# Performance work log

Measured on AMD Instinct MI355X. Metric: run time of the kernel, lower is better.

## Reference

```python
import jax, jax.numpy as jnp
import numpy as np

B, S, D, H = 2, 2048, 1024, 16
DK = D // H  # 64, per-head key/value dim


def setup_inputs() -> dict:
    key = jax.random.key(0)
    ks = jax.random.split(key, 8)
    q = jax.random.normal(ks[0], (B, S, D), dtype=jnp.float32)
    k = jax.random.normal(ks[1], (B, S, D), dtype=jnp.float32)
    v = jax.random.normal(ks[2], (B, S, D), dtype=jnp.float32)
    # per-head projection weights, initialized like torch.randn in the original
    W_q = jax.random.normal(ks[3], (H, D, DK), dtype=jnp.float32)
    W_k = jax.random.normal(ks[4], (H, D, DK), dtype=jnp.float32)
    W_v = jax.random.normal(ks[5], (H, D, DK), dtype=jnp.float32)
    # output nn.Linear(H*DK, D): weight [D, H*DK], bias [D]
    bound = 1.0 / np.sqrt(H * DK)
    W_o = jax.random.uniform(ks[6], (D, H * DK), dtype=jnp.float32, minval=-bound, maxval=bound)
    b_o = jax.random.uniform(ks[7], (D,), dtype=jnp.float32, minval=-bound, maxval=bound)
    return {"q": q, "k": k, "v": v, "W_q": W_q, "W_k": W_k, "W_v": W_v, "W_o": W_o, "b_o": b_o}


def reference(q, k, v, W_q, W_k, W_v, W_o, b_o):
    dk = W_q.shape[-1]
    # batched per-head projections (replaces the Python loop over heads)
    qh = jnp.einsum('bsd,hdk->bhsk', q, W_q)  # [B,H,S,DK]
    kh = jnp.einsum('bsd,hdk->bhsk', k, W_k)
    vh = jnp.einsum('bsd,hdk->bhsk', v, W_v)
    scale = jnp.asarray(np.sqrt(dk), qh.dtype)
    scores = jnp.einsum('bhsk,bhtk->bhst', qh, kh) / scale  # [B,H,S,S]
    attn = jax.nn.softmax(scores, axis=-1)
    ctx = jnp.einsum('bhst,bhtk->bhsk', attn, vh)  # [B,H,S,DK]
    # concat heads along feature dim (matches torch.cat(..., dim=2))
    b, h, s, d = ctx.shape
    ctx = ctx.transpose(0, 2, 1, 3).reshape(b, s, h * d)  # [B,S,H*DK]
    return ctx @ W_o.T + b_o  # [B,S,D]
```

## Files before the change

kernel.cpp:

```cpp
#include <hip/hip_runtime.h>
#include <math.h>

#define B_ 2
#define S_ 2048
#define D_ 1024
#define H_ 16
#define ATTN_C 0.18033688011f

typedef unsigned short ushort_t;
typedef __attribute__((ext_vector_type(8))) short short8;
typedef __attribute__((ext_vector_type(4))) short short4v;
typedef __attribute__((ext_vector_type(4))) float f32x4;
typedef __attribute__((ext_vector_type(2))) float f32x2;
typedef __attribute__((ext_vector_type(16))) float f32x16;
typedef __attribute__((ext_vector_type(4))) unsigned int uint4v;

#define MFMA(A, B, C) __builtin_amdgcn_mfma_f32_32x32x16_bf16((A), (B), (C), 0, 0, 0)
#define Z16 {0.f,0.f,0.f,0.f,0.f,0.f,0.f,0.f,0.f,0.f,0.f,0.f,0.f,0.f,0.f,0.f}

__device__ __forceinline__ ushort_t bf16rn(float x) {
    unsigned int u = __builtin_bit_cast(unsigned int, x);
    u += 0x7FFFu + ((u >> 16) & 1u);
    return (ushort_t)(u >> 16);
}
__device__ __forceinline__ float bf16tof(ushort_t h) {
    return __builtin_bit_cast(float, (unsigned int)h << 16);
}
__device__ __forceinline__ unsigned cvtpk(float lo, float hi) {
    unsigned r;
    asm("v_cvt_pk_bf16_f32 %0, %1, %2" : "=v"(r) : "v"(lo), "v"(hi));
    return r;
}
__device__ __forceinline__ void gload16(const void* g, void* l) {
    __builtin_amdgcn_global_load_lds(
        (const __attribute__((address_space(1))) unsigned int*)(unsigned long long)g,
        (__attribute__((address_space(3))) unsigned int*)(unsigned int)(unsigned long long)l,
        16, 0, 0);
}

__global__ __launch_bounds__(256) void cvtx_kernel(
    const float* __restrict__ Xq, const float* __restrict__ Xk,
    const float* __restrict__ Xv,
    ushort_t* __restrict__ Xh, ushort_t* __restrict__ Xl)
{
    const int pr = blockIdx.y;
    const float* X = pr == 0 ? Xq : pr == 1 ? Xk : Xv;
    const size_t idx = ((size_t)blockIdx.x * 256 + threadIdx.x) * 8;
    f32x4 v0 = *(const f32x4*)(X + idx);
    f32x4 v1 = *(const f32x4*)(X + idx + 4);
    float f[8] = {v0.x, v0.y, v0.z, v0.w, v1.x, v1.y, v1.z, v1.w};
    short8 hi, lo;
#pragma unroll
    for (int i = 0; i < 8; ++i) {
        ushort_t hh = bf16rn(f[i]);
        hi[i] = (short)hh;
        lo[i] = (short)bf16rn(f[i] - bf16tof(hh));
    }
    const size_t base = (size_t)pr * 2 * S_ * D_;
    *(short8*)(Xh + base + idx) = hi;
    if (pr < 2) *(short8*)(Xl + base + idx) = lo;
}

__global__ __launch_bounds__(256) void cvtw_kernel(
    const float* __restrict__ Wq, const float* __restrict__ Wk,
    const float* __restrict__ Wv,
    ushort_t* __restrict__ wqh, ushort_t* __restrict__ wql,
    ushort_t* __restrict__ wkh, ushort_t* __restrict__ wkl,
    ushort_t* __restrict__ wvh)
{
    __shared__ float T[64][68];
    const int dt = blockIdx.x, h = blockIdx.y, mat = blockIdx.z;
    const int tid = threadIdx.x;
    const float* W = mat == 0 ? Wq : mat == 1 ? Wk : Wv;
    const float* Wb = W + ((size_t)h * 1024 + dt * 64) * 64;
#pragma unroll
    for (int u = 0; u < 4; ++u) {
        int idx = tid + u * 256;
        int d = idx >> 4, c4 = idx & 15;
        f32x4 v = *(const f32x4*)(Wb + (size_t)d * 64 + c4 * 4);
        T[d][c4 * 4 + 0] = v.x; T[d][c4 * 4 + 1] = v.y;
        T[d][c4 * 4 + 2] = v.z; T[d][c4 * 4 + 3] = v.w;
    }
    __syncthreads();
    ushort_t* oh = mat == 0 ? wqh : mat == 1 ? wkh : wvh;
    ushort_t* ol = mat == 0 ? wql : mat == 1 ? wkl : nullptr;
#pragma unroll
    for (int u = 0; u < 4; ++u) {
        int idx = tid + u * 256;
        int n = idx >> 4, c4 = idx & 15;
        float v0 = T[c4 * 4 + 0][n], v1 = T[c4 * 4 + 1][n];
        float v2 = T[c4 * 4 + 2][n], v3 = T[c4 * 4 + 3][n];
        ushort_t h0 = bf16rn(v0), h1 = bf16rn(v1), h2 = bf16rn(v2), h3 = bf16rn(v3);
        size_t off = ((size_t)h * 64 + n) * 1024 + dt * 64 + c4 * 4;
        short4v hv = {(short)h0, (short)h1, (short)h2, (short)h3};
        *(short4v*)(oh + off) = hv;
        if (ol) {
            short4v lv = {(short)bf16rn(v0 - bf16tof(h0)), (short)bf16rn(v1 - bf16tof(h1)),
                          (short)bf16rn(v2 - bf16tof(h2)), (short)bf16rn(v3 - bf16tof(h3))};
            *(short4v*)(ol + off) = lv;
        }
    }
}

__global__ __launch_bounds__(256) void cvtwo_kernel(
    const float* __restrict__ Wo, ushort_t* __restrict__ wob)
{
    size_t idx = (size_t)blockIdx.x * 256 + threadIdx.x;
    f32x4 v = *(const f32x4*)(Wo + idx * 4);
    short4v o = {(short)bf16rn(v.x), (short)bf16rn(v.y),
                 (short)bf16rn(v.z), (short)bf16rn(v.w)};
    *(short4v*)(wob + idx * 4) = o;
}

__global__ __launch_bounds__(256, 2) void proj_kernel(
    const ushort_t* __restrict__ Xh, const ushort_t* __restrict__ Xl,
    const ushort_t* __restrict__ Wh_q, const ushort_t* __restrict__ Wl_q,
    const ushort_t* __restrict__ Wh_k, const ushort_t* __restrict__ Wl_k,
    const ushort_t* __restrict__ Wh_v,
    ushort_t* __restrict__ Oq_h, ushort_t* __restrict__ Oq_l,
    ushort_t* __restrict__ Ok_h, ushort_t* __restrict__ Ok_l,
    ushort_t* __restrict__ Ov)
{
    __shared__ __align__(16) ushort_t Xs[128 * 128];
    __shared__ __align__(16) ushort_t Ws[128 * 128];
    const int tid = threadIdx.x;
    const int wv = tid >> 6, lane = tid & 63;
    const int lo32 = lane & 31, g = lane >> 5;
    const int wm = wv >> 1, wn = wv & 1;
    const int lrow = lane >> 4, lg = lane & 15;
    const int m0 = blockIdx.x * 128;
    const int n0 = blockIdx.y * 128;
    const int pr = blockIdx.z >> 1, b = blockIdx.z & 1;
    const bool split = (pr != 2);
    const ushort_t* Whp = pr == 0 ? Wh_q : pr == 1 ? Wh_k : Wh_v;
    const ushort_t* Wlp = pr == 0 ? Wl_q : pr == 1 ? Wl_k : Wh_v;
    const ushort_t* Xhb = Xh + ((size_t)(pr * 2 + b) * S_ + m0) * D_;
    const ushort_t* Xlb = Xl + ((size_t)(pr * 2 + b) * S_ + m0) * D_;
    f32x16 a00 = Z16, a01 = Z16, a10 = Z16, a11 = Z16;

    for (int d0 = 0; d0 < D_; d0 += 64) {
        __syncthreads();
#pragma unroll
        for (int u = 0; u < 8; ++u) {
            int row = u * 16 + wv * 4 + lrow;
            int gs = lg ^ (row & 15);
            int half = gs >> 3, c8 = gs & 7;
            const ushort_t* srcX = ((half && split) ? Xlb : Xhb) + (size_t)row * D_ + d0 + c8 * 8;
            gload16(srcX, (char*)Xs + (u * 16 + wv * 4) * 256);
            const ushort_t* srcW = ((half && split) ? Wlp : Whp) + (size_t)(n0 + row) * 1024 + d0 + c8 * 8;
            gload16(srcW, (char*)Ws + (u * 16 + wv * 4) * 256);
        }
        __syncthreads();
#pragma unroll
        for (int ks = 0; ks < 4; ++ks) {
            int coff = ks * 16 + g * 8;
            int r0 = wm * 64 + lo32, r1 = r0 + 32;
            int c0 = wn * 64 + lo32, c1 = c0 + 32;
            short8 a0h = *(const short8*)&Xs[(r0 * 128 + coff) ^ ((r0 & 15) << 3)];
            short8 a1h = *(const short8*)&Xs[(r1 * 128 + coff) ^ ((r1 & 15) << 3)];
            short8 b0h = *(const short8*)&Ws[(c0 * 128 + coff) ^ ((c0 & 15) << 3)];
            short8 b1h = *(const short8*)&Ws[(c1 * 128 + coff) ^ ((c1 & 15) << 3)];
            a00 = MFMA(a0h, b0h, a00);
            a01 = MFMA(a0h, b1h, a01);
            a10 = MFMA(a1h, b0h, a10);
            a11 = MFMA(a1h, b1h, a11);
            if (split) {
                short8 a0l = *(const short8*)&Xs[(r0 * 128 + 64 + coff) ^ ((r0 & 15) << 3)];
                short8 a1l = *(const short8*)&Xs[(r1 * 128 + 64 + coff) ^ ((r1 & 15) << 3)];
                short8 b0l = *(const short8*)&Ws[(c0 * 128 + 64 + coff) ^ ((c0 & 15) << 3)];
                short8 b1l = *(const short8*)&Ws[(c1 * 128 + 64 + coff) ^ ((c1 & 15) << 3)];
                a00 = MFMA(a0h, b0l, a00); a00 = MFMA(a0l, b0h, a00);
                a01 = MFMA(a0h, b1l, a01); a01 = MFMA(a0l, b1h, a01);
                a10 = MFMA(a1h, b0l, a10); a10 = MFMA(a1l, b0h, a10);
                a11 = MFMA(a1h, b1l, a11); a11 = MFMA(a1l, b1h, a11);
            }
        }
    }
    ushort_t* OH = pr == 0 ? Oq_h : pr == 1 ? Ok_h : Ov;
    ushort_t* OL = pr == 0 ? Oq_l : pr == 1 ? Ok_l : Ov;
    const bool qscale = (pr == 0);
#define PROJ_STORE(ACC, MT, NT)                                               \
    _Pragma("unroll")                                                         \
    for (int r = 0; r < 16; ++r) {                                            \
        int s_loc = m0 + wm * 64 + (MT) * 32 + (r & 3) + 8 * (r >> 2) + 4 * g;\
        int col = n0 + wn * 64 + (NT) * 32 + lo32;                            \
        int hh_ = col >> 6, nn = col & 63;                                    \
        float val = ACC[r];                                                   \
        if (qscale) val *= ATTN_C;                                            \
        size_t off = (((size_t)b * H_ + hh_) * S_ + s_loc) * 64 + nn;         \
        if (split) {                                                          \
            ushort_t hv = bf16rn(val);                                        \
            OH[off] = hv;                                                     \
            OL[off] = bf16rn(val - bf16tof(hv));                              \
        } else OH[off] = bf16rn(val);                                         \
    }
    PROJ_STORE(a00, 0, 0)
    PROJ_STORE(a01, 0, 1)
    PROJ_STORE(a10, 1, 0)
    PROJ_STORE(a11, 1, 1)
#undef PROJ_STORE
}

__global__ __launch_bounds__(256, 4) void attn_kernel(
    const ushort_t* __restrict__ qh_h, const ushort_t* __restrict__ qh_l,
    const ushort_t* __restrict__ kh_h, const ushort_t* __restrict__ kh_l,
    const ushort_t* __restrict__ vh, ushort_t* __restrict__ Opart,
    float* __restrict__ Ml)
{
    __shared__ __align__(16) char smem[32768];
    ushort_t* Ks = (ushort_t*)smem;
    ushort_t* Vt = (ushort_t*)(smem + 16384);
    const int tid = threadIdx.x;
    const int wv = tid >> 6, lane = tid & 63;
    const int lo32 = lane & 31, g = lane >> 5;
    const int lrow = lane >> 4, lg = lane & 15;
    const int s0 = blockIdx.x * 128;
    const int h = blockIdx.y;
    const int b = blockIdx.z >> 1, sp = blockIdx.z & 1;
    const size_t bhs = ((size_t)b * H_ + h) * S_ * 64;

    const ushort_t* Qrh = qh_h + bhs + (size_t)(s0 + wv * 32 + lo32) * 64;
    const ushort_t* Qrl = qh_l + bhs + (size_t)(s0 + wv * 32 + lo32) * 64;
    short8 qfh[4], qfl[4];
#pragma unroll
    for (int ks = 0; ks < 4; ++ks) {
        qfh[ks] = *(const short8*)(Qrh + ks * 16 + g * 8);
        qfl[ks] = *(const short8*)(Qrl + ks * 16 + g * 8);
    }
    const ushort_t* Kgh = kh_h + bhs;
    const ushort_t* Kgl = kh_l + bhs;
    const ushort_t* Vg = vh + bhs;

    f32x16 o0 = Z16, o1 = Z16;
    float mrun = -3.0e38f, lrun = 0.0f;
    const int kvbeg = sp * (S_ / 2), kvend = kvbeg + (S_ / 2);

    for (int kv0 = kvbeg; kv0 < kvend; kv0 += 64) {
        __syncthreads();
#pragma unroll
        for (int u = 0; u < 4; ++u) {
            int row = wv * 16 + u * 4 + lrow;
            int gs = lg ^ (row & 15);
            int half = gs >> 3, c8 = gs & 7;
            const ushort_t* src = (half ? Kgl : Kgh) + (size_t)(kv0 + row) * 64 + c8 * 8;
            gload16(src, (char*)Ks + (wv * 16 + u * 4) * 256);
        }
        {
            int kvp = tid & 31, d8 = tid >> 5;
            const ushort_t* vp = Vg + (size_t)(kv0 + 2 * kvp) * 64 + d8 * 8;
            short8 va = *(const short8*)(vp);
            short8 vb = *(const short8*)(vp + 64);
#pragma unroll
            for (int i = 0; i < 8; ++i) {
                int d = d8 * 8 + i;
                unsigned wrd = ((unsigned)(ushort_t)vb[i] << 16) | (ushort_t)va[i];
                *(unsigned*)&Vt[(d * 64 + 2 * kvp) ^ ((d & 7) << 3)] = wrd;
            }
        }
        __syncthreads();
#pragma unroll
        for (int ch = 0; ch < 2; ++ch) {
            int kvb = ch * 32;
            f32x16 st = Z16;
#pragma unroll
            for (int ks = 0; ks < 4; ++ks) {
                int krow = kvb + lo32;
                int base = krow * 128 + ks * 16 + g * 8;
                int sw = (krow & 15) << 3;
                short8 kfh = *(const short8*)&Ks[base ^ sw];
                short8 kfl = *(const short8*)&Ks[(base + 64) ^ sw];
                st = MFMA(kfh, qfh[ks], st);
                st = MFMA(kfh, qfl[ks], st);
                st = MFMA(kfl, qfh[ks], st);
            }
            float t0 = fmaxf(fmaxf(st[0], st[1]), st[2]);
            float t1 = fmaxf(fmaxf(st[3], st[4]), st[5]);
            float t2 = fmaxf(fmaxf(st[6], st[7]), st[8]);
            float t3 = fmaxf(fmaxf(st[9], st[10]), st[11]);
            float t4 = fmaxf(fmaxf(st[12], st[13]), st[14]);
            float cmax = fmaxf(fmaxf(fmaxf(t0, t1), t2),
                               fmaxf(fmaxf(t3, t4), st[15]));
            cmax = fmaxf(cmax, __shfl_xor(cmax, 32));
            if (!__all(cmax <= mrun)) {
                float mnew = fmaxf(mrun, cmax);
                float corr = __builtin_amdgcn_exp2f(mrun - mnew);
                lrun *= corr;
#pragma unroll
                for (int r = 0; r < 16; ++r) { o0[r] *= corr; o1[r] *= corr; }
                mrun = mnew;
            }
            float p[16];
            float ls = 0.f;
#pragma unroll
            for (int r = 0; r < 16; ++r) {
                p[r] = __builtin_amdgcn_exp2f(st[r] - mrun);
                ls += p[r];
            }
            lrun += ls;
#pragma unroll
            for (int ks2 = 0; ks2 < 2; ++ks2) {
                int rr = ks2 * 8;
                unsigned w0 = cvtpk(p[rr + 0], p[rr + 1]);
                unsigned w1 = cvtpk(p[rr + 2], p[rr + 3]);
                unsigned w2 = cvtpk(p[rr + 4], p[rr + 5]);
                unsigned w3 = cvtpk(p[rr + 6], p[rr + 7]);
                asm("v_permlane32_swap_b32 %0, %1" : "+v"(w0), "+v"(w2));
                asm("v_permlane32_swap_b32 %0, %1" : "+v"(w1), "+v"(w3));
                uint4v pw = {w0, w1, w2, w3};
                short8 pfrag = __builtin_bit_cast(short8, pw);
                int kvf = kvb + ks2 * 16 + g * 8;
                int vsw = (lo32 & 7) << 3;
                short8 vf0 = *(const short8*)&Vt[(lo32 * 64 + kvf) ^ vsw];
                short8 vf1 = *(const short8*)&Vt[((lo32 + 32) * 64 + kvf) ^ vsw];
                o0 = MFMA(vf0, pfrag, o0);
                o1 = MFMA(vf1, pfrag, o1);
            }
        }
    }
    lrun += __shfl_xor(lrun, 32);
    __syncthreads();
    float* Oe = ((float*)smem) + wv * 2048;
#pragma unroll
    for (int r = 0; r < 16; ++r) {
        int dd = (r & 3) + 8 * (r >> 2) + 4 * g;
        int qsw = (lo32 & 7) << 2;
        Oe[(lo32 * 64 + dd) ^ qsw] = o0[r];
        Oe[(lo32 * 64 + 32 + dd) ^ qsw] = o1[r];
    }
    const size_t orow = (size_t)sp * (B_ * H_ * S_) + ((size_t)b * H_ + h) * S_ + s0 + wv * 32;
#pragma unroll
    for (int rep = 0; rep < 8; ++rep) {
        int idx = lane + rep * 64;
        int qq = idx >> 4, d4 = idx & 15;
        f32x4 ov = *(const f32x4*)&Oe[(qq * 64 + d4 * 4) ^ ((qq & 7) << 2)];
        short4v pk4 = {(short)bf16rn(ov.x), (short)bf16rn(ov.y),
                       (short)bf16rn(ov.z), (short)bf16rn(ov.w)};
        *(short4v*)(Opart + (orow + qq) * 64 + d4 * 4) = pk4;
    }
    if (g == 0) {
        f32x2 ml = {mrun, lrun};
        *(f32x2*)(Ml + (orow + lo32) * 2) = ml;
    }
}

__global__ __launch_bounds__(256) void merge_kernel(
    const ushort_t* __restrict__ Opart, const float* __restrict__ Ml,
    ushort_t* __restrict__ ctxb)
{
    const int NROW = B_ * H_ * S_;
    int gidx = blockIdx.x * 256 + threadIdx.x;
    int row = gidx >> 3, d8 = (gidx & 7) * 8;
    f32x2 ml0 = *(const f32x2*)(Ml + (size_t)row * 2);
    f32x2 ml1 = *(const f32x2*)(Ml + ((size_t)NROW + row) * 2);
    float M = fmaxf(ml0.x, ml1.x);
    float w0 = __builtin_amdgcn_exp2f(ml0.x - M);
    float w1 = __builtin_amdgcn_exp2f(ml1.x - M);
    float inv = 1.f / (ml0.y * w0 + ml1.y * w1);
    w0 *= inv; w1 *= inv;
    short8 a = *(const short8*)(Opart + (size_t)row * 64 + d8);
    short8 c = *(const short8*)(Opart + ((size_t)NROW + row) * 64 + d8);
    short8 o;
#pragma unroll
    for (int i = 0; i < 8; ++i) {
        float f = bf16tof((ushort_t)a[i]) * w0 + bf16tof((ushort_t)c[i]) * w1;
        o[i] = (short)bf16rn(f);
    }
    int bb = row >> 15, hh = (row >> 11) & 15, s = row & 2047;
    *(short8*)(ctxb + ((size_t)bb * S_ + s) * D_ + hh * 64 + d8) = o;
}

__global__ __launch_bounds__(128, 2) void outproj_kernel(
    const ushort_t* __restrict__ ctxb, const ushort_t* __restrict__ wob,
    const float* __restrict__ bo, float* __restrict__ Out)
{
    __shared__ __align__(16) ushort_t Cs[128 * 128];
    __shared__ __align__(16) ushort_t Ws2[64 * 128];
    const int tid = threadIdx.x;
    const int wv = tid >> 6, lane = tid & 63;
    const int lo32 = lane & 31, g = lane >> 5;
    const int lrow = lane >> 4, lg = lane & 15;
    const int n0 = blockIdx.x * 64;
    const int m0 = blockIdx.y * 128;
    f32x16 a00 = Z16, a01 = Z16, a10 = Z16, a11 = Z16;
    for (int k0 = 0; k0 < D_; k0 += 128) {
        __syncthreads();
#pragma unroll
        for (int u = 0; u < 16; ++u) {
            int row = u * 8 + wv * 4 + lrow;
            int gs = lg ^ (row & 15);
            const ushort_t* src = ctxb + (size_t)(m0 + row) * D_ + k0 + gs * 8;
            gload16(src, (char*)Cs + (u * 8 + wv * 4) * 256);
        }
#pragma unroll
        for (int u = 0; u < 8; ++u) {
            int row = u * 8 + wv * 4 + lrow;
            int gs = lg ^ (row & 15);
            const ushort_t* src = wob + (size_t)(n0 + row) * D_ + k0 + gs * 8;
            gload16(src, (char*)Ws2 + (u * 8 + wv * 4) * 256);
        }
        __syncthreads();
#pragma unroll
        for (int ks = 0; ks < 8; ++ks) {
            int coff = ks * 16 + g * 8;
            int r0 = wv * 64 + lo32, r1 = r0 + 32;
            int n1 = lo32 + 32;
            short8 A0 = *(const short8*)&Cs[(r0 * 128 + coff) ^ ((r0 & 15) << 3)];
            short8 A1 = *(const short8*)&Cs[(r1 * 128 + coff) ^ ((r1 & 15) << 3)];
            short8 B0 = *(const short8*)&Ws2[(lo32 * 128 + coff) ^ ((lo32 & 15) << 3)];
            short8 B1 = *(const short8*)&Ws2[(n1 * 128 + coff) ^ ((n1 & 15) << 3)];
            a00 = MFMA(A0, B0, a00);
            a01 = MFMA(A0, B1, a01);
            a10 = MFMA(A1, B0, a10);
            a11 = MFMA(A1, B1, a11);
        }
    }
    float b0v = bo[n0 + lo32], b1v = bo[n0 + 32 + lo32];
#define OUT_STORE(ACC, MT, NT, BV)                                          \
    _Pragma("unroll")                                                       \
    for (int r = 0; r < 16; ++r) {                                          \
        int m = m0 + wv * 64 + (MT) * 32 + (r & 3) + 8 * (r >> 2) + 4 * g;  \
        int n = n0 + (NT) * 32 + lo32;                                      \
        Out[(size_t)m * D_ + n] = ACC[r] + (BV);                            \
    }
    OUT_STORE(a00, 0, 0, b0v)
    OUT_STORE(a01, 0, 1, b1v)
    OUT_STORE(a10, 1, 0, b0v)
    OUT_STORE(a11, 1, 1, b1v)
#undef OUT_STORE
}

extern "C" void kernel_launch(void* const* d_in, const int* in_sizes, int n_in,
                              void* d_out, int out_size, void* d_ws,
                              size_t ws_size, hipStream_t stream)
{
    const float* q = (const float*)d_in[0];
    const float* k = (const float*)d_in[1];
    const float* v = (const float*)d_in[2];
    const float* W_q = (const float*)d_in[3];
    const float* W_k = (const float*)d_in[4];
    const float* W_v = (const float*)d_in[5];
    const float* W_o = (const float*)d_in[6];
    const float* b_o = (const float*)d_in[7];
    float* out = (float*)d_out;

    ushort_t* wqt_h = (ushort_t*)d_ws;
    ushort_t* wqt_l = wqt_h + (1 << 20);
    ushort_t* wkt_h = wqt_l + (1 << 20);
    ushort_t* wkt_l = wkt_h + (1 << 20);
    ushort_t* wvt_h = wkt_l + (1 << 20);
    ushort_t* wob   = wvt_h + (1 << 20);
    ushort_t* qh_h  = wob + (1 << 20);
    ushort_t* qh_l  = qh_h + (1 << 22);
    ushort_t* kh_h  = qh_l + (1 << 22);
    ushort_t* kh_l  = kh_h + (1 << 22);
    ushort_t* vhp   = kh_l + (1 << 22);
    ushort_t* Xh    = vhp + (1 << 22);
    ushort_t* Xl    = Xh + 3 * (1 << 22);
    ushort_t* ctxb  = Xh;
    ushort_t* Opart = Xl;
    float*    Ml    = (float*)(Xl + 2 * (size_t)(B_ * H_ * S_) * 64);

    cvtx_kernel<<<dim3(2048, 3), 256, 0, stream>>>(q, k, v, Xh, Xl);
    cvtw_kernel<<<dim3(16, 16, 3), 256, 0, stream>>>(
        W_q, W_k, W_v, wqt_h, wqt_l, wkt_h, wkt_l, wvt_h);
    cvtwo_kernel<<<1024, 256, 0, stream>>>(W_o, wob);
    proj_kernel<<<dim3(16, 8, 6), 256, 0, stream>>>(
        Xh, Xl, wqt_h, wqt_l, wkt_h, wkt_l, wvt_h,
        qh_h, qh_l, kh_h, kh_l, vhp);
    attn_kernel<<<dim3(16, 16, 4), 256, 0, stream>>>(
        qh_h, qh_l, kh_h, kh_l, vhp, Opart, Ml);
    merge_kernel<<<2048, 256, 0, stream>>>(Opart, Ml, ctxb);
    outproj_kernel<<<dim3(16, 32), 128, 0, stream>>>(ctxb, wob, b_o, out);
}
```

Before: 224.3 us.

## Widen attention tiles, pre-transpose V in projection, skip negligible score chunks

The projection kernel now writes V directly in a transposed [d][s] layout, so the attention kernel can load it with async 16-byte copies instead of transposing it through registers. Each wave now handles 64 query rows (two 32-row fragments) against 128-key tiles. Each key fragment is reused across two query fragments, and synchronisation is amortised over more work, at the cost of fewer blocks per CU and more registers. A chunk is skipped when its high-part-only scores are all at least 142 below the running max. Otherwise the low-part correction MFMAs run only for the query fragments that need them, avoiding exp and PV work whose contribution underflows.

```diff
diff --git a/kernel.cpp b/kernel.cpp
--- a/kernel.cpp
+++ b/kernel.cpp
@@ -119,7 +119,7 @@
     const ushort_t* __restrict__ Wh_v,
     ushort_t* __restrict__ Oq_h, ushort_t* __restrict__ Oq_l,
     ushort_t* __restrict__ Ok_h, ushort_t* __restrict__ Ok_l,
-    ushort_t* __restrict__ Ov)
+    ushort_t* __restrict__ Ovt)
 {
     __shared__ __align__(16) ushort_t Xs[128 * 128];
     __shared__ __align__(16) ushort_t Ws[128 * 128];
@@ -176,8 +176,8 @@
             }
         }
     }
-    ushort_t* OH = pr == 0 ? Oq_h : pr == 1 ? Ok_h : Ov;
-    ushort_t* OL = pr == 0 ? Oq_l : pr == 1 ? Ok_l : Ov;
+    ushort_t* OH = pr == 0 ? Oq_h : pr == 1 ? Ok_h : Ovt;
+    ushort_t* OL = pr == 0 ? Oq_l : pr == 1 ? Ok_l : Ovt;
     const bool qscale = (pr == 0);
 #define PROJ_STORE(ACC, MT, NT)                                               \
     _Pragma("unroll")                                                         \
@@ -187,12 +187,15 @@
         int hh_ = col >> 6, nn = col & 63;                                    \
         float val = ACC[r];                                                   \
         if (qscale) val *= ATTN_C;                                            \
-        size_t off = (((size_t)b * H_ + hh_) * S_ + s_loc) * 64 + nn;         \
         if (split) {                                                          \
+            size_t off = (((size_t)b * H_ + hh_) * S_ + s_loc) * 64 + nn;     \
             ushort_t hv = bf16rn(val);                                        \
             OH[off] = hv;                                                     \
             OL[off] = bf16rn(val - bf16tof(hv));                              \
-        } else OH[off] = bf16rn(val);                                         \
+        } else {                                                              \
+            size_t offt = (((size_t)b * H_ + hh_) * 64 + nn) * S_ + s_loc;    \
+            OH[offt] = bf16rn(val);                                           \
+        }                                                                     \
     }
     PROJ_STORE(a00, 0, 0)
     PROJ_STORE(a01, 0, 1)
@@ -201,133 +204,203 @@
 #undef PROJ_STORE
 }
 
-__global__ __launch_bounds__(256, 4) void attn_kernel(
+__global__ __launch_bounds__(256, 2) void attn_kernel(
     const ushort_t* __restrict__ qh_h, const ushort_t* __restrict__ qh_l,
     const ushort_t* __restrict__ kh_h, const ushort_t* __restrict__ kh_l,
-    const ushort_t* __restrict__ vh, ushort_t* __restrict__ Opart,
+    const ushort_t* __restrict__ vt, ushort_t* __restrict__ Opart,
     float* __restrict__ Ml)
 {
-    __shared__ __align__(16) char smem[32768];
+    __shared__ __align__(16) char smem[49152];
     ushort_t* Ks = (ushort_t*)smem;
-    ushort_t* Vt = (ushort_t*)(smem + 16384);
+    ushort_t* Vt = (ushort_t*)(smem + 32768);
     const int tid = threadIdx.x;
     const int wv = tid >> 6, lane = tid & 63;
     const int lo32 = lane & 31, g = lane >> 5;
     const int lrow = lane >> 4, lg = lane & 15;
-    const int s0 = blockIdx.x * 128;
+    const int s0 = blockIdx.x * 256;
     const int h = blockIdx.y;
     const int b = blockIdx.z >> 1, sp = blockIdx.z & 1;
     const size_t bhs = ((size_t)b * H_ + h) * S_ * 64;
 
-    const ushort_t* Qrh = qh_h + bhs + (size_t)(s0 + wv * 32 + lo32) * 64;
-    const ushort_t* Qrl = qh_l + bhs + (size_t)(s0 + wv * 32 + lo32) * 64;
-    short8 qfh[4], qfl[4];
-#pragma unroll
-    for (int ks = 0; ks < 4; ++ks) {
-        qfh[ks] = *(const short8*)(Qrh + ks * 16 + g * 8);
-        qfl[ks] = *(const short8*)(Qrl + ks * 16 + g * 8);
+    short8 qfh[2][4], qfl[2][4];
+#pragma unroll
+    for (int c = 0; c < 2; ++c) {
+        const ushort_t* Qrh = qh_h + bhs + (size_t)(s0 + wv * 64 + c * 32 + lo32) * 64;
+        const ushort_t* Qrl = qh_l + bhs + (size_t)(s0 + wv * 64 + c * 32 + lo32) * 64;
+#pragma unroll
+        for (int ks = 0; ks < 4; ++ks) {
+            qfh[c][ks] = *(const short8*)(Qrh + ks * 16 + g * 8);
+            qfl[c][ks] = *(const short8*)(Qrl + ks * 16 + g * 8);
+        }
     }
     const ushort_t* Kgh = kh_h + bhs;
     const ushort_t* Kgl = kh_l + bhs;
-    const ushort_t* Vg = vh + bhs;
-
-    f32x16 o0 = Z16, o1 = Z16;
-    float mrun = -3.0e38f, lrun = 0.0f;
+    const ushort_t* Vtg = vt + ((size_t)b * H_ + h) * 64 * S_;
+
+    f32x16 o00 = Z16, o01 = Z16, o10 = Z16, o11 = Z16;
+    float mrun0 = -3.0e38f, mrun1 = -3.0e38f;
+    float lrun0 = 0.f, lrun1 = 0.f;
     const int kvbeg = sp * (S_ / 2), kvend = kvbeg + (S_ / 2);
 
-    for (int kv0 = kvbeg; kv0 < kvend; kv0 += 64) {
+    for (int kv0 = kvbeg; kv0 < kvend; kv0 += 128) {
         __syncthreads();
 #pragma unroll
-        for (int u = 0; u < 4; ++u) {
-            int row = wv * 16 + u * 4 + lrow;
+        for (int u = 0; u < 8; ++u) {
+            int row = u * 16 + wv * 4 + lrow;
             int gs = lg ^ (row & 15);
             int half = gs >> 3, c8 = gs & 7;
             const ushort_t* src = (half ? Kgl : Kgh) + (size_t)(kv0 + row) * 64 + c8 * 8;
-            gload16(src, (char*)Ks + (wv * 16 + u * 4) * 256);
-        }
-        {
-            int kvp = tid & 31, d8 = tid >> 5;
-            const ushort_t* vp = Vg + (size_t)(kv0 + 2 * kvp) * 64 + d8 * 8;
-            short8 va = *(const short8*)(vp);
-            short8 vb = *(const short8*)(vp + 64);
-#pragma unroll
-            for (int i = 0; i < 8; ++i) {
-                int d = d8 * 8 + i;
-                unsigned wrd = ((unsigned)(ushort_t)vb[i] << 16) | (ushort_t)va[i];
-                *(unsigned*)&Vt[(d * 64 + 2 * kvp) ^ ((d & 7) << 3)] = wrd;
+            gload16(src, (char*)Ks + (u * 16 + wv * 4) * 256);
+        }
+#pragma unroll
+        for (int u = 0; u < 4; ++u) {
+            int d = u * 16 + wv * 4 + lrow;
+            int gsrc = (lg & 8) | ((lg & 7) ^ (d & 7));
+            const ushort_t* src = Vtg + (size_t)d * S_ + kv0 + gsrc * 8;
+            gload16(src, (char*)Vt + (u * 16 + wv * 4) * 256);
+        }
+        __syncthreads();
+#pragma unroll 1
+        for (int ch = 0; ch < 4; ++ch) {
+            const int kvb = ch * 32;
+            const int krow = kvb + lo32;
+            const int ksw = (krow & 15) << 3;
+            short8 kfh0 = *(const short8*)&Ks[(krow * 128 + 0 * 16 + g * 8) ^ ksw];
+            short8 kfh1 = *(const short8*)&Ks[(krow * 128 + 1 * 16 + g * 8) ^ ksw];
+            short8 kfh2 = *(const short8*)&Ks[(krow * 128 + 2 * 16 + g * 8) ^ ksw];
+            short8 kfh3 = *(const short8*)&Ks[(krow * 128 + 3 * 16 + g * 8) ^ ksw];
+            f32x16 st0 = Z16, st1 = Z16;
+            st0 = MFMA(kfh0, qfh[0][0], st0);  st1 = MFMA(kfh0, qfh[1][0], st1);
+            st0 = MFMA(kfh1, qfh[0][1], st0);  st1 = MFMA(kfh1, qfh[1][1], st1);
+            st0 = MFMA(kfh2, qfh[0][2], st0);  st1 = MFMA(kfh2, qfh[1][2], st1);
+            st0 = MFMA(kfh3, qfh[0][3], st0);  st1 = MFMA(kfh3, qfh[1][3], st1);
+            float cm0 = fmaxf(fmaxf(fmaxf(st0[0], st0[1]), fmaxf(st0[2], st0[3])),
+                              fmaxf(fmaxf(st0[4], st0[5]), fmaxf(st0[6], st0[7])));
+            cm0 = fmaxf(cm0, fmaxf(fmaxf(fmaxf(st0[8], st0[9]), fmaxf(st0[10], st0[11])),
+                                   fmaxf(fmaxf(st0[12], st0[13]), fmaxf(st0[14], st0[15]))));
+            float cm1 = fmaxf(fmaxf(fmaxf(st1[0], st1[1]), fmaxf(st1[2], st1[3])),
+                              fmaxf(fmaxf(st1[4], st1[5]), fmaxf(st1[6], st1[7])));
+            cm1 = fmaxf(cm1, fmaxf(fmaxf(fmaxf(st1[8], st1[9]), fmaxf(st1[10], st1[11])),
+                                   fmaxf(fmaxf(st1[12], st1[13]), fmaxf(st1[14], st1[15]))));
+            cm0 = fmaxf(cm0, __shfl_xor(cm0, 32));
+            cm1 = fmaxf(cm1, __shfl_xor(cm1, 32));
+            const bool need0 = !__all(cm0 <= mrun0 - 142.f);
+            const bool need1 = !__all(cm1 <= mrun1 - 142.f);
+            if (!need0 && !need1) continue;
+            short8 kfl0 = *(const short8*)&Ks[(krow * 128 + 64 + 0 * 16 + g * 8) ^ ksw];
+            short8 kfl1 = *(const short8*)&Ks[(krow * 128 + 64 + 1 * 16 + g * 8) ^ ksw];
+            short8 kfl2 = *(const short8*)&Ks[(krow * 128 + 64 + 2 * 16 + g * 8) ^ ksw];
+            short8 kfl3 = *(const short8*)&Ks[(krow * 128 + 64 + 3 * 16 + g * 8) ^ ksw];
+            unsigned pw0[8], pw1[8];
+            if (need0) {
+                st0 = MFMA(kfh0, qfl[0][0], st0);  st0 = MFMA(kfl0, qfh[0][0], st0);
+                st0 = MFMA(kfh1, qfl[0][1], st0);  st0 = MFMA(kfl1, qfh[0][1], st0);
+                st0 = MFMA(kfh2, qfl[0][2], st0);  st0 = MFMA(kfl2, qfh[0][2], st0);
+                st0 = MFMA(kfh3, qfl[0][3], st0);  st0 = MFMA(kfl3, qfh[0][3], st0);
+                float cme = fmaxf(fmaxf(fmaxf(st0[0], st0[1]), fmaxf(st0[2], st0[3])),
+                                  fmaxf(fmaxf(st0[4], st0[5]), fmaxf(st0[6], st0[7])));
+                cme = fmaxf(cme, fmaxf(fmaxf(fmaxf(st0[8], st0[9]), fmaxf(st0[10], st0[11])),
+                                       fmaxf(fmaxf(st0[12], st0[13]), fmaxf(st0[14], st0[15]))));
+                cme = fmaxf(cme, __shfl_xor(cme, 32));
+                if (!__all(cme <= mrun0)) {
+                    float mnew = fmaxf(mrun0, cme);
+                    float corr = __builtin_amdgcn_exp2f(mrun0 - mnew);
+                    lrun0 *= corr;
+#pragma unroll
+                    for (int r = 0; r < 16; ++r) { o00[r] *= corr; o01[r] *= corr; }
+                    mrun0 = mnew;
+                }
+                float p[16], ls = 0.f;
+#pragma unroll
+                for (int r = 0; r < 16; ++r) {
+                    p[r] = __builtin_amdgcn_exp2f(st0[r] - mrun0);
+                    ls += p[r];
+                }
+                lrun0 += ls;
+#pragma unroll
+                for (int ks2 = 0; ks2 < 2; ++ks2) {
+                    unsigned w0 = cvtpk(p[ks2 * 8 + 0], p[ks2 * 8 + 1]);
+                    unsigned w1 = cvtpk(p[ks2 * 8 + 2], p[ks2 * 8 + 3]);
+                    unsigned w2 = cvtpk(p[ks2 * 8 + 4], p[ks2 * 8 + 5]);
+                    unsigned w3 = cvtpk(p[ks2 * 8 + 6], p[ks2 * 8 + 7]);
+                    asm("v_permlane32_swap_b32 %0, %1" : "+v"(w0), "+v"(w2));
+                    asm("v_permlane32_swap_b32 %0, %1" : "+v"(w1), "+v"(w3));
+                    pw0[ks2 * 4 + 0] = w0; pw0[ks2 * 4 + 1] = w1;
+                    pw0[ks2 * 4 + 2] = w2; pw0[ks2 * 4 + 3] = w3;
+                }
             }
-        }
-        __syncthreads();
-#pragma unroll
-        for (int ch = 0; ch < 2; ++ch) {
-            int kvb = ch * 32;
-            f32x16 st = Z16;
-#pragma unroll
-            for (int ks = 0; ks < 4; ++ks) {
-                int krow = kvb + lo32;
-                int base = krow * 128 + ks * 16 + g * 8;
-                int sw = (krow & 15) << 3;
-                short8 kfh = *(const short8*)&Ks[base ^ sw];
-                short8 kfl = *(const short8*)&Ks[(base + 64) ^ sw];
-                st = MFMA(kfh, qfh[ks], st);
-                st = MFMA(kfh, qfl[ks], st);
-                st = MFMA(kfl, qfh[ks], st);
+            if (need1) {
+                st1 = MFMA(kfh0, qfl[1][0], st1);  st1 = MFMA(kfl0, qfh[1][0], st1);
+                st1 = MFMA(kfh1, qfl[1][1], st1);  st1 = MFMA(kfl1, qfh[1][1], st1);
+                st1 = MFMA(kfh2, qfl[1][2], st1);  st1 = MFMA(kfl2, qfh[1][2], st1);
+                st1 = MFMA(kfh3, qfl[1][3], st1);  st1 = MFMA(kfl3, qfh[1][3], st1);
+                float cme = fmaxf(fmaxf(fmaxf(st1[0], st1[1]), fmaxf(st1[2], st1[3])),
+                                  fmaxf(fmaxf(st1[4], st1[5]), fmaxf(st1[6], st1[7])));
+                cme = fmaxf(cme, fmaxf(fmaxf(fmaxf(st1[8], st1[9]), fmaxf(st1[10], st1[11])),
+                                       fmaxf(fmaxf(st1[12], st1[13]), fmaxf(st1[14], st1[15]))));
+                cme = fmaxf(cme, __shfl_xor(cme, 32));
+                if (!__all(cme <= mrun1)) {
+                    float mnew = fmaxf(mrun1, cme);
+                    float corr = __builtin_amdgcn_exp2f(mrun1 - mnew);
+                    lrun1 *= corr;
+#pragma unroll
+                    for (int r = 0; r < 16; ++r) { o10[r] *= corr; o11[r] *= corr; }
+                    mrun1 = mnew;
+                }
+                float p[16], ls = 0.f;
+#pragma unroll
+                for (int r = 0; r < 16; ++r) {
+                    p[r] = __builtin_amdgcn_exp2f(st1[r] - mrun1);
+                    ls += p[r];
+                }
+                lrun1 += ls;
+#pragma unroll
+                for (int ks2 = 0; ks2 < 2; ++ks2) {
+                    unsigned w0 = cvtpk(p[ks2 * 8 + 0], p[ks2 * 8 + 1]);
+                    unsigned w1 = cvtpk(p[ks2 * 8 + 2], p[ks2 * 8 + 3]);
+                    unsigned w2 = cvtpk(p[ks2 * 8 + 4], p[ks2 * 8 + 5]);
+                    unsigned w3 = cvtpk(p[ks2 * 8 + 6], p[ks2 * 8 + 7]);
+                    asm("v_permlane32_swap_b32 %0, %1" : "+v"(w0), "+v"(w2));
+                    asm("v_permlane32_swap_b32 %0, %1" : "+v"(w1), "+v"(w3));
+                    pw1[ks2 * 4 + 0] = w0; pw1[ks2 * 4 + 1] = w1;
+                    pw1[ks2 * 4 + 2] = w2; pw1[ks2 * 4 + 3] = w3;
+                }
             }
-            float t0 = fmaxf(fmaxf(st[0], st[1]), st[2]);
-            float t1 = fmaxf(fmaxf(st[3], st[4]), st[5]);
-            float t2 = fmaxf(fmaxf(st[6], st[7]), st[8]);
-            float t3 = fmaxf(fmaxf(st[9], st[10]), st[11]);
-            float t4 = fmaxf(fmaxf(st[12], st[13]), st[14]);
-            float cmax = fmaxf(fmaxf(fmaxf(t0, t1), t2),
-                               fmaxf(fmaxf(t3, t4), st[15]));
-            cmax = fmaxf(cmax, __shfl_xor(cmax, 32));
-            if (!__all(cmax <= mrun)) {
-                float mnew = fmaxf(mrun, cmax);
-                float corr = __builtin_amdgcn_exp2f(mrun - mnew);
-                lrun *= corr;
-#pragma unroll
-                for (int r = 0; r < 16; ++r) { o0[r] *= corr; o1[r] *= corr; }
-                mrun = mnew;
-            }
-            float p[16];
-            float ls = 0.f;
-#pragma unroll
-            for (int r = 0; r < 16; ++r) {
-                p[r] = __builtin_amdgcn_exp2f(st[r] - mrun);
-                ls += p[r];
-            }
-            lrun += ls;
 #pragma unroll
             for (int ks2 = 0; ks2 < 2; ++ks2) {
-                int rr = ks2 * 8;
-                unsigned w0 = cvtpk(p[rr + 0], p[rr + 1]);
-                unsigned w1 = cvtpk(p[rr + 2], p[rr + 3]);
-                unsigned w2 = cvtpk(p[rr + 4], p[rr + 5]);
-                unsigned w3 = cvtpk(p[rr + 6], p[rr + 7]);
-                asm("v_permlane32_swap_b32 %0, %1" : "+v"(w0), "+v"(w2));
-                asm("v_permlane32_swap_b32 %0, %1" : "+v"(w1), "+v"(w3));
-                uint4v pw = {w0, w1, w2, w3};
-                short8 pfrag = __builtin_bit_cast(short8, pw);
                 int kvf = kvb + ks2 * 16 + g * 8;
                 int vsw = (lo32 & 7) << 3;
-                short8 vf0 = *(const short8*)&Vt[(lo32 * 64 + kvf) ^ vsw];
-                short8 vf1 = *(const short8*)&Vt[((lo32 + 32) * 64 + kvf) ^ vsw];
-                o0 = MFMA(vf0, pfrag, o0);
-                o1 = MFMA(vf1, pfrag, o1);
+                short8 vf0 = *(const short8*)&Vt[(lo32 * 128 + kvf) ^ vsw];
+                short8 vf1 = *(const short8*)&Vt[((lo32 + 32) * 128 + kvf) ^ vsw];
+                if (need0) {
+                    uint4v a = {pw0[ks2 * 4 + 0], pw0[ks2 * 4 + 1],
+                                pw0[ks2 * 4 + 2], pw0[ks2 * 4 + 3]};
+                    short8 pf = __builtin_bit_cast(short8, a);
+                    o00 = MFMA(vf0, pf, o00);
+                    o01 = MFMA(vf1, pf, o01);
+                }
+                if (need1) {
+                    uint4v a = {pw1[ks2 * 4 + 0], pw1[ks2 * 4 + 1],
+                                pw1[ks2 * 4 + 2], pw1[ks2 * 4 + 3]};
+                    short8 pf = __builtin_bit_cast(short8, a);
+                    o10 = MFMA(vf0, pf, o10);
+                    o11 = MFMA(vf1, pf, o11);
+                }
             }
         }
     }
-    lrun += __shfl_xor(lrun, 32);
+    lrun0 += __shfl_xor(lrun0, 32);
+    lrun1 += __shfl_xor(lrun1, 32);
     __syncthreads();
     float* Oe = ((float*)smem) + wv * 2048;
+    const size_t orowb = (size_t)sp * (B_ * H_ * S_) + ((size_t)b * H_ + h) * S_ + s0 + wv * 64;
 #pragma unroll
     for (int r = 0; r < 16; ++r) {
         int dd = (r & 3) + 8 * (r >> 2) + 4 * g;
         int qsw = (lo32 & 7) << 2;
-        Oe[(lo32 * 64 + dd) ^ qsw] = o0[r];
-        Oe[(lo32 * 64 + 32 + dd) ^ qsw] = o1[r];
-    }
-    const size_t orow = (size_t)sp * (B_ * H_ * S_) + ((size_t)b * H_ + h) * S_ + s0 + wv * 32;
+        Oe[(lo32 * 64 + dd) ^ qsw] = o00[r];
+        Oe[(lo32 * 64 + 32 + dd) ^ qsw] = o01[r];
+    }
 #pragma unroll
     for (int rep = 0; rep < 8; ++rep) {
         int idx = lane + rep * 64;
@@ -335,11 +408,32 @@
         f32x4 ov = *(const f32x4*)&Oe[(qq * 64 + d4 * 4) ^ ((qq & 7) << 2)];
         short4v pk4 = {(short)bf16rn(ov.x), (short)bf16rn(ov.y),
                        (short)bf16rn(ov.z), (short)bf16rn(ov.w)};
-        *(short4v*)(Opart + (orow + qq) * 64 + d4 * 4) = pk4;
+        *(short4v*)(Opart + (orowb + qq) * 64 + d4 * 4) = pk4;
     }
     if (g == 0) {
-        f32x2 ml = {mrun, lrun};
-        *(f32x2*)(Ml + (orow + lo32) * 2) = ml;
+        f32x2 ml = {mrun0, lrun0};
+        *(f32x2*)(Ml + (orowb + lo32) * 2) = ml;
+    }
+    __builtin_amdgcn_s_waitcnt(0);
+#pragma unroll
+    for (int r = 0; r < 16; ++r) {
+        int dd = (r & 3) + 8 * (r >> 2) + 4 * g;
+        int qsw = (lo32 & 7) << 2;
+        Oe[(lo32 * 64 + dd) ^ qsw] = o10[r];
+        Oe[(lo32 * 64 + 32 + dd) ^ qsw] = o11[r];
+    }
+#pragma unroll
+    for (int rep = 0; rep < 8; ++rep) {
+        int idx = lane + rep * 64;
+        int qq = idx >> 4, d4 = idx & 15;
+        f32x4 ov = *(const f32x4*)&Oe[(qq * 64 + d4 * 4) ^ ((qq & 7) << 2)];
+        short4v pk4 = {(short)bf16rn(ov.x), (short)bf16rn(ov.y),
+                       (short)bf16rn(ov.z), (short)bf16rn(ov.w)};
+        *(short4v*)(Opart + (orowb + 32 + qq) * 64 + d4 * 4) = pk4;
+    }
+    if (g == 0) {
+        f32x2 ml = {mrun1, lrun1};
+        *(f32x2*)(Ml + (orowb + 32 + lo32) * 2) = ml;
     }
 }
 
@@ -453,8 +547,8 @@
     ushort_t* qh_l  = qh_h + (1 << 22);
     ushort_t* kh_h  = qh_l + (1 << 22);
     ushort_t* kh_l  = kh_h + (1 << 22);
-    ushort_t* vhp   = kh_l + (1 << 22);
-    ushort_t* Xh    = vhp + (1 << 22);
+    ushort_t* vtp   = kh_l + (1 << 22);
+    ushort_t* Xh    = vtp + (1 << 22);
     ushort_t* Xl    = Xh + 3 * (1 << 22);
     ushort_t* ctxb  = Xh;
     ushort_t* Opart = Xl;
@@ -466,9 +560,9 @@
     cvtwo_kernel<<<1024, 256, 0, stream>>>(W_o, wob);
     proj_kernel<<<dim3(16, 8, 6), 256, 0, stream>>>(
         Xh, Xl, wqt_h, wqt_l, wkt_h, wkt_l, wvt_h,
-        qh_h, qh_l, kh_h, kh_l, vhp);
-    attn_kernel<<<dim3(16, 16, 4), 256, 0, stream>>>(
-        qh_h, qh_l, kh_h, kh_l, vhp, Opart, Ml);
+        qh_h, qh_l, kh_h, kh_l, vtp);
+    attn_kernel<<<dim3(8, 16, 4), 256, 0, stream>>>(
+        qh_h, qh_l, kh_h, kh_l, vtp, Opart, Ml);
     merge_kernel<<<2048, 256, 0, stream>>>(Opart, Ml, ctxb);
     outproj_kernel<<<dim3(16, 32), 128, 0, stream>>>(ctxb, wob, b_o, out);
 }
```

New measurement: 229.7 us. 1.02x slower.

## Transpose V in projection, stream K from global, skip negligible attention blocks

Applied to the files above, without the earlier changes.

The projection kernel now writes V pre-transposed, staged through shared memory, so the attention kernel can bulk-load V tiles with async copies instead of transposing them element by element. K fragments are read straight from global memory into registers, which frees the K shared-memory buffer and allows 128-wide KV tiles. Each 32-key chunk first computes a high-part-only score and skips the remaining MFMAs, exp and PV work when its max is far below the running max; a second check after the full score skips chunks contributing below about 2^-30. Occupancy hint drops from 4 to 3 blocks. The skip is a data-dependent approximation with bounded error, and uncached global K loads may add latency.

```diff
diff --git a/kernel.cpp b/kernel.cpp
--- a/kernel.cpp
+++ b/kernel.cpp
@@ -119,7 +119,7 @@
     const ushort_t* __restrict__ Wh_v,
     ushort_t* __restrict__ Oq_h, ushort_t* __restrict__ Oq_l,
     ushort_t* __restrict__ Ok_h, ushort_t* __restrict__ Ok_l,
-    ushort_t* __restrict__ Ov)
+    ushort_t* __restrict__ Ovt)
 {
     __shared__ __align__(16) ushort_t Xs[128 * 128];
     __shared__ __align__(16) ushort_t Ws[128 * 128];
@@ -176,9 +176,10 @@
             }
         }
     }
-    ushort_t* OH = pr == 0 ? Oq_h : pr == 1 ? Ok_h : Ov;
-    ushort_t* OL = pr == 0 ? Oq_l : pr == 1 ? Ok_l : Ov;
-    const bool qscale = (pr == 0);
+    if (split) {
+        ushort_t* OH = pr == 0 ? Oq_h : Ok_h;
+        ushort_t* OL = pr == 0 ? Oq_l : Ok_l;
+        const bool qscale = (pr == 0);
 #define PROJ_STORE(ACC, MT, NT)                                               \
     _Pragma("unroll")                                                         \
     for (int r = 0; r < 16; ++r) {                                            \
@@ -188,28 +189,51 @@
         float val = ACC[r];                                                   \
         if (qscale) val *= ATTN_C;                                            \
         size_t off = (((size_t)b * H_ + hh_) * S_ + s_loc) * 64 + nn;         \
-        if (split) {                                                          \
-            ushort_t hv = bf16rn(val);                                        \
-            OH[off] = hv;                                                     \
-            OL[off] = bf16rn(val - bf16tof(hv));                              \
-        } else OH[off] = bf16rn(val);                                         \
-    }
-    PROJ_STORE(a00, 0, 0)
-    PROJ_STORE(a01, 0, 1)
-    PROJ_STORE(a10, 1, 0)
-    PROJ_STORE(a11, 1, 1)
+        ushort_t hv = bf16rn(val);                                            \
+        OH[off] = hv;                                                         \
+        OL[off] = bf16rn(val - bf16tof(hv));                                  \
+    }
+        PROJ_STORE(a00, 0, 0)
+        PROJ_STORE(a01, 0, 1)
+        PROJ_STORE(a10, 1, 0)
+        PROJ_STORE(a11, 1, 1)
 #undef PROJ_STORE
-}
-
-__global__ __launch_bounds__(256, 4) void attn_kernel(
+    } else {
+        __syncthreads();
+        ushort_t* T = Xs;
+#define VT_PUT(ACC, MT, NT)                                                   \
+    _Pragma("unroll")                                                         \
+    for (int r = 0; r < 16; ++r) {                                            \
+        int s_loc = wm * 64 + (MT) * 32 + (r & 3) + 8 * (r >> 2) + 4 * g;     \
+        int col   = wn * 64 + (NT) * 32 + lo32;                               \
+        T[col * 128 + (s_loc ^ ((col & 15) << 3))] = bf16rn(ACC[r]);          \
+    }
+        VT_PUT(a00, 0, 0)
+        VT_PUT(a01, 0, 1)
+        VT_PUT(a10, 1, 0)
+        VT_PUT(a11, 1, 1)
+#undef VT_PUT
+        __syncthreads();
+#pragma unroll
+        for (int u = 0; u < 8; ++u) {
+            int idx = tid + u * 256;
+            int col = idx >> 4, ch = idx & 15;
+            short8 v8 = *(const short8*)&T[col * 128 + ((ch * 8) ^ ((col & 15) << 3))];
+            int gn = n0 + col;
+            size_t orow = ((size_t)b * H_ + (gn >> 6)) * 64 + (gn & 63);
+            *(short8*)(Ovt + orow * S_ + m0 + ch * 8) = v8;
+        }
+    }
+}
+
+__global__ __launch_bounds__(256, 3) void attn_kernel(
     const ushort_t* __restrict__ qh_h, const ushort_t* __restrict__ qh_l,
     const ushort_t* __restrict__ kh_h, const ushort_t* __restrict__ kh_l,
-    const ushort_t* __restrict__ vh, ushort_t* __restrict__ Opart,
+    const ushort_t* __restrict__ vt, ushort_t* __restrict__ Opart,
     float* __restrict__ Ml)
 {
     __shared__ __align__(16) char smem[32768];
-    ushort_t* Ks = (ushort_t*)smem;
-    ushort_t* Vt = (ushort_t*)(smem + 16384);
+    ushort_t* Vt = (ushort_t*)smem;
     const int tid = threadIdx.x;
     const int wv = tid >> 6, lane = tid & 63;
     const int lo32 = lane & 31, g = lane >> 5;
@@ -229,97 +253,99 @@
     }
     const ushort_t* Kgh = kh_h + bhs;
     const ushort_t* Kgl = kh_l + bhs;
-    const ushort_t* Vg = vh + bhs;
+    const ushort_t* Vtg = vt + ((size_t)b * H_ + h) * 64 * S_;
 
     f32x16 o0 = Z16, o1 = Z16;
-    float mrun = -3.0e38f, lrun = 0.0f;
-    const int kvbeg = sp * (S_ / 2), kvend = kvbeg + (S_ / 2);
-
-    for (int kv0 = kvbeg; kv0 < kvend; kv0 += 64) {
+    float mrun = -3.0e38f, lrun = 0.f;
+    const int kvbeg = sp * (S_ / 2);
+
+#define MAX16(ST)                                                             \
+    fmaxf(fmaxf(fmaxf(fmaxf(ST[0], ST[1]), ST[2]),                            \
+                fmaxf(fmaxf(ST[3], ST[4]), ST[5])),                           \
+          fmaxf(fmaxf(fmaxf(ST[6], ST[7]), fmaxf(ST[8], ST[9])),              \
+                fmaxf(fmaxf(fmaxf(ST[10], ST[11]), ST[12]),                   \
+                      fmaxf(fmaxf(ST[13], ST[14]), ST[15]))))
+
+    for (int t = 0; t < 8; ++t) {
+        const int kv0 = kvbeg + t * 128;
         __syncthreads();
 #pragma unroll
         for (int u = 0; u < 4; ++u) {
-            int row = wv * 16 + u * 4 + lrow;
-            int gs = lg ^ (row & 15);
-            int half = gs >> 3, c8 = gs & 7;
-            const ushort_t* src = (half ? Kgl : Kgh) + (size_t)(kv0 + row) * 64 + c8 * 8;
-            gload16(src, (char*)Ks + (wv * 16 + u * 4) * 256);
-        }
-        {
-            int kvp = tid & 31, d8 = tid >> 5;
-            const ushort_t* vp = Vg + (size_t)(kv0 + 2 * kvp) * 64 + d8 * 8;
-            short8 va = *(const short8*)(vp);
-            short8 vb = *(const short8*)(vp + 64);
-#pragma unroll
-            for (int i = 0; i < 8; ++i) {
-                int d = d8 * 8 + i;
-                unsigned wrd = ((unsigned)(ushort_t)vb[i] << 16) | (ushort_t)va[i];
-                *(unsigned*)&Vt[(d * 64 + 2 * kvp) ^ ((d & 7) << 3)] = wrd;
-            }
-        }
-        __syncthreads();
-#pragma unroll
-        for (int ch = 0; ch < 2; ++ch) {
-            int kvb = ch * 32;
+            int d = u * 16 + wv * 4 + lrow;
+            int gsrc = (lg & 8) | ((lg & 7) ^ (d & 7));
+            const ushort_t* src = Vtg + (size_t)d * S_ + kv0 + gsrc * 8;
+            gload16(src, (char*)Vt + (u * 16 + wv * 4) * 256);
+        }
+        __syncthreads();
+#pragma unroll 1
+        for (int ch = 0; ch < 4; ++ch) {
+            const int ci = t * 4 + ch;
+            const ushort_t* pkh = Kgh + (size_t)(kvbeg + ci * 32 + lo32) * 64 + g * 8;
+            const ushort_t* pkl = Kgl + (size_t)(kvbeg + ci * 32 + lo32) * 64 + g * 8;
+            short8 kh0 = *(const short8*)(pkh);
+            short8 kh1 = *(const short8*)(pkh + 16);
+            short8 kh2 = *(const short8*)(pkh + 32);
+            short8 kh3 = *(const short8*)(pkh + 48);
+            short8 kl0 = *(const short8*)(pkl);
+            short8 kl1 = *(const short8*)(pkl + 16);
+            short8 kl2 = *(const short8*)(pkl + 32);
+            short8 kl3 = *(const short8*)(pkl + 48);
             f32x16 st = Z16;
-#pragma unroll
-            for (int ks = 0; ks < 4; ++ks) {
-                int krow = kvb + lo32;
-                int base = krow * 128 + ks * 16 + g * 8;
-                int sw = (krow & 15) << 3;
-                short8 kfh = *(const short8*)&Ks[base ^ sw];
-                short8 kfl = *(const short8*)&Ks[(base + 64) ^ sw];
-                st = MFMA(kfh, qfh[ks], st);
-                st = MFMA(kfh, qfl[ks], st);
-                st = MFMA(kfl, qfh[ks], st);
-            }
-            float t0 = fmaxf(fmaxf(st[0], st[1]), st[2]);
-            float t1 = fmaxf(fmaxf(st[3], st[4]), st[5]);
-            float t2 = fmaxf(fmaxf(st[6], st[7]), st[8]);
-            float t3 = fmaxf(fmaxf(st[9], st[10]), st[11]);
-            float t4 = fmaxf(fmaxf(st[12], st[13]), st[14]);
-            float cmax = fmaxf(fmaxf(fmaxf(t0, t1), t2),
-                               fmaxf(fmaxf(t3, t4), st[15]));
-            cmax = fmaxf(cmax, __shfl_xor(cmax, 32));
-            if (!__all(cmax <= mrun)) {
-                float mnew = fmaxf(mrun, cmax);
+            st = MFMA(kh0, qfh[0], st);
+            st = MFMA(kh1, qfh[1], st);
+            st = MFMA(kh2, qfh[2], st);
+            st = MFMA(kh3, qfh[3], st);
+            float cm = MAX16(st);
+            cm = fmaxf(cm, __shfl_xor(cm, 32));
+            if (!__any(cm > mrun - 64.f)) continue;
+            st = MFMA(kh0, qfl[0], st);  st = MFMA(kl0, qfh[0], st);
+            st = MFMA(kh1, qfl[1], st);  st = MFMA(kl1, qfh[1], st);
+            st = MFMA(kh2, qfl[2], st);  st = MFMA(kl2, qfh[2], st);
+            st = MFMA(kh3, qfl[3], st);  st = MFMA(kl3, qfh[3], st);
+            float cme = MAX16(st);
+            cme = fmaxf(cme, __shfl_xor(cme, 32));
+            if (!__any(cme > mrun - 30.f)) continue;
+            if (__any(cme > mrun)) {
+                float mnew = fmaxf(mrun, cme);
                 float corr = __builtin_amdgcn_exp2f(mrun - mnew);
                 lrun *= corr;
 #pragma unroll
                 for (int r = 0; r < 16; ++r) { o0[r] *= corr; o1[r] *= corr; }
                 mrun = mnew;
             }
-            float p[16];
-            float ls = 0.f;
+            float p[16], ls = 0.f;
 #pragma unroll
             for (int r = 0; r < 16; ++r) {
                 p[r] = __builtin_amdgcn_exp2f(st[r] - mrun);
                 ls += p[r];
             }
             lrun += ls;
+            const int kvb = ch * 32;
+            const int vsw = (lo32 & 7) << 3;
 #pragma unroll
             for (int ks2 = 0; ks2 < 2; ++ks2) {
-                int rr = ks2 * 8;
-                unsigned w0 = cvtpk(p[rr + 0], p[rr + 1]);
-                unsigned w1 = cvtpk(p[rr + 2], p[rr + 3]);
-                unsigned w2 = cvtpk(p[rr + 4], p[rr + 5]);
-                unsigned w3 = cvtpk(p[rr + 6], p[rr + 7]);
+                unsigned w0 = cvtpk(p[ks2 * 8 + 0], p[ks2 * 8 + 1]);
+                unsigned w1 = cvtpk(p[ks2 * 8 + 2], p[ks2 * 8 + 3]);
+                unsigned w2 = cvtpk(p[ks2 * 8 + 4], p[ks2 * 8 + 5]);
+                unsigned w3 = cvtpk(p[ks2 * 8 + 6], p[ks2 * 8 + 7]);
                 asm("v_permlane32_swap_b32 %0, %1" : "+v"(w0), "+v"(w2));
                 asm("v_permlane32_swap_b32 %0, %1" : "+v"(w1), "+v"(w3));
                 uint4v pw = {w0, w1, w2, w3};
-                short8 pfrag = __builtin_bit_cast(short8, pw);
+                short8 pf = __builtin_bit_cast(short8, pw);
                 int kvf = kvb + ks2 * 16 + g * 8;
-                int vsw = (lo32 & 7) << 3;
-                short8 vf0 = *(const short8*)&Vt[(lo32 * 64 + kvf) ^ vsw];
-                short8 vf1 = *(const short8*)&Vt[((lo32 + 32) * 64 + kvf) ^ vsw];
-                o0 = MFMA(vf0, pfrag, o0);
-                o1 = MFMA(vf1, pfrag, o1);
+                short8 vf0 = *(const short8*)&Vt[(lo32 * 128 + kvf) ^ vsw];
+                short8 vf1 = *(const short8*)&Vt[((lo32 + 32) * 128 + kvf) ^ vsw];
+                o0 = MFMA(vf0, pf, o0);
+                o1 = MFMA(vf1, pf, o1);
             }
         }
     }
+#undef MAX16
+
     lrun += __shfl_xor(lrun, 32);
     __syncthreads();
     float* Oe = ((float*)smem) + wv * 2048;
+    const size_t orowb = (size_t)sp * (B_ * H_ * S_) + ((size_t)b * H_ + h) * S_ + s0 + wv * 32;
 #pragma unroll
     for (int r = 0; r < 16; ++r) {
         int dd = (r & 3) + 8 * (r >> 2) + 4 * g;
@@ -327,7 +353,6 @@
         Oe[(lo32 * 64 + dd) ^ qsw] = o0[r];
         Oe[(lo32 * 64 + 32 + dd) ^ qsw] = o1[r];
     }
-    const size_t orow = (size_t)sp * (B_ * H_ * S_) + ((size_t)b * H_ + h) * S_ + s0 + wv * 32;
 #pragma unroll
     for (int rep = 0; rep < 8; ++rep) {
         int idx = lane + rep * 64;
@@ -335,11 +360,11 @@
         f32x4 ov = *(const f32x4*)&Oe[(qq * 64 + d4 * 4) ^ ((qq & 7) << 2)];
         short4v pk4 = {(short)bf16rn(ov.x), (short)bf16rn(ov.y),
                        (short)bf16rn(ov.z), (short)bf16rn(ov.w)};
-        *(short4v*)(Opart + (orow + qq) * 64 + d4 * 4) = pk4;
+        *(short4v*)(Opart + (orowb + qq) * 64 + d4 * 4) = pk4;
     }
     if (g == 0) {
         f32x2 ml = {mrun, lrun};
-        *(f32x2*)(Ml + (orow + lo32) * 2) = ml;
+        *(f32x2*)(Ml + (orowb + lo32) * 2) = ml;
     }
 }
 
@@ -453,8 +478,8 @@
     ushort_t* qh_l  = qh_h + (1 << 22);
     ushort_t* kh_h  = qh_l + (1 << 22);
     ushort_t* kh_l  = kh_h + (1 << 22);
-    ushort_t* vhp   = kh_l + (1 << 22);
-    ushort_t* Xh    = vhp + (1 << 22);
+    ushort_t* vtp   = kh_l + (1 << 22);
+    ushort_t* Xh    = vtp + (1 << 22);
     ushort_t* Xl    = Xh + 3 * (1 << 22);
     ushort_t* ctxb  = Xh;
     ushort_t* Opart = Xl;
@@ -466,9 +491,9 @@
     cvtwo_kernel<<<1024, 256, 0, stream>>>(W_o, wob);
     proj_kernel<<<dim3(16, 8, 6), 256, 0, stream>>>(
         Xh, Xl, wqt_h, wqt_l, wkt_h, wkt_l, wvt_h,
-        qh_h, qh_l, kh_h, kh_l, vhp);
+        qh_h, qh_l, kh_h, kh_l, vtp);
     attn_kernel<<<dim3(16, 16, 4), 256, 0, stream>>>(
-        qh_h, qh_l, kh_h, kh_l, vhp, Opart, Ml);
+        qh_h, qh_l, kh_h, kh_l, vtp, Opart, Ml);
     merge_kernel<<<2048, 256, 0, stream>>>(Opart, Ml, ctxb);
     outproj_kernel<<<dim3(16, 32), 128, 0, stream>>>(ctxb, wob, b_o, out);
 }
```

Result: slower. 299.8 us (+33.6%).
